# Kernel optimization log

Measured on AMD Instinct MI355X. Metric: run time of the kernel, lower is better.

Reference implementation:

```python
import jax, jax.numpy as jnp
import numpy as np

INPUT_SIZE = 128
HIDDEN_SIZE = 1024
OUTPUT_SIZE = 64
E_PROP = 0.8
E_SIZE = int(E_PROP * HIDDEN_SIZE)  # 819
I_SIZE = HIDDEN_SIZE - E_SIZE       # 205


def _make_mask():
    # rows of [+1]*E_SIZE + [-1]*I_SIZE, zero diagonal (no self-connection)
    row = np.concatenate([np.ones(E_SIZE), -np.ones(I_SIZE)]).astype(np.float32)
    mask = np.tile(row, (HIDDEN_SIZE, 1))
    np.fill_diagonal(mask, 0.0)
    return jnp.asarray(mask)


def setup_inputs() -> dict:
    key = jax.random.key(0)
    ks = jax.random.split(key, 8)
    T, B = 512, 64
    scale = 1.0 / np.sqrt(HIDDEN_SIZE)
    x = jax.random.normal(ks[0], (T, B, INPUT_SIZE), dtype=jnp.float32)
    w_ih = jax.random.normal(ks[1], (HIDDEN_SIZE, INPUT_SIZE), dtype=jnp.float32) / np.sqrt(INPUT_SIZE)
    b_ih = jax.random.uniform(ks[2], (HIDDEN_SIZE,), minval=-scale, maxval=scale, dtype=jnp.float32)
    w_hh = jax.random.normal(ks[3], (HIDDEN_SIZE, HIDDEN_SIZE), dtype=jnp.float32) * scale
    # mimic reset_parameters: shrink excitatory columns by e_size/i_size ratio
    w_hh = w_hh.at[:, :E_SIZE].divide(E_SIZE / I_SIZE)
    b_hh = jax.random.uniform(ks[4], (HIDDEN_SIZE,), minval=-scale, maxval=scale, dtype=jnp.float32)
    w_fc = jax.random.normal(ks[5], (OUTPUT_SIZE, E_SIZE), dtype=jnp.float32) / np.sqrt(E_SIZE)
    b_fc = jax.random.uniform(ks[6], (OUTPUT_SIZE,), minval=-scale, maxval=scale, dtype=jnp.float32)
    # NOTE: RNN.__init__ hard-codes alpha = 1 regardless of the value passed in.
    alpha = jnp.array([1.0], dtype=jnp.float32)
    mask = _make_mask()
    return {"x": x, "w_ih": w_ih, "b_ih": b_ih, "w_hh": w_hh, "b_hh": b_hh,
            "w_fc": w_fc, "b_fc": b_fc, "alpha": alpha, "mask": mask}


def reference(x, w_ih, b_ih, w_hh, b_hh, w_fc, b_fc, alpha, mask):
    # x: (T, B, I). Precompute input projection for all timesteps (one big GEMM).
    inp_proj = jnp.einsum('tbi,hi->tbh', x, w_ih) + b_ih  # (T, B, H)
    # effective E-I weight: sign-constrained, zero diagonal; constant across steps
    eff_w = jnp.abs(w_hh) * mask                           # (H, H)
    a = alpha[0]
    B = x.shape[1]
    state0 = jnp.zeros((B, HIDDEN_SIZE), dtype=x.dtype)
    out0 = jnp.zeros((B, HIDDEN_SIZE), dtype=x.dtype)

    def step(carry, u_t):
        state, output = carry
        total = u_t + output @ eff_w.T + b_hh             # (B, H)
        state = a * (total - state) + state               # alpha blend (sigma_rec = 0)
        output = jnp.tanh(state)
        return (state, output), output

    _, rnn_activity = jax.lax.scan(step, (state0, out0), inp_proj)  # (T, B, H)
    rnn_e = rnn_activity[:, :, :E_SIZE]                   # excitatory readout only
    out = jnp.einsum('tbe,oe->tbo', rnn_e, w_fc) + b_fc   # (T, B, O)
    return out, rnn_activity
```

## Files before the change

kernel.cpp:

```cpp
#include <hip/hip_runtime.h>
#include <cmath>

#define T_STEPS 512
#define BATCH   64
#define HID     1024
#define INSZ    128
#define ESZ     819
#define OSZ     64

#define WS_EFFW   0
#define WS_WIHT   1048576
#define WS_HIST   1179648
#define WS_BADJ   34734080
#define WS_WFCP   34742272

typedef float f32x4 __attribute__((ext_vector_type(4)));

__global__ void prep_effw(const float* __restrict__ w_hh, const float* __restrict__ mask,
                          float* __restrict__ eff) {
    const int i = (blockIdx.x * 256 + threadIdx.x) * 4;
    const float4 w = *(const float4*)(w_hh + i);
    const float4 m = *(const float4*)(mask + i);
    float4 r;
    r.x = fabsf(w.x) * m.x; r.y = fabsf(w.y) * m.y;
    r.z = fabsf(w.z) * m.z; r.w = fabsf(w.w) * m.w;
    *(float4*)(eff + i) = r;
}

__global__ void prep_wihT(const float* __restrict__ w_ih, float* __restrict__ w_ihT) {
    const int idx = blockIdx.x * 256 + threadIdx.x;
    const int i = idx >> 10, h = idx & 1023;
    w_ihT[idx] = w_ih[h * INSZ + i];
}

__global__ void prep_wfc(const float* __restrict__ w_fc, const float* __restrict__ b_fc,
                         float* __restrict__ w_fcp, float* __restrict__ badj) {
    __shared__ float red[256];
    const int o = blockIdx.x, tid = threadIdx.x;
    float s = 0.f;
    for (int e = tid; e < 820; e += 256) {
        const float w = (e < ESZ) ? w_fc[o * ESZ + e] : 0.f;
        w_fcp[o * 820 + e] = w;
        s += w;
    }
    red[tid] = s;
    __syncthreads();
    for (int st = 128; st; st >>= 1) {
        if (tid < st) red[tid] += red[tid + st];
        __syncthreads();
    }
    if (tid == 0) badj[o] = b_fc[o] - 2.0f * red[0];
}

__global__ void inp_proj(const float* __restrict__ x, const float* __restrict__ w_ihT,
                         const float* __restrict__ b_ih, float* __restrict__ u) {
    __shared__ float xs[INSZ * 64];
    const int t = blockIdx.x, tid = threadIdx.x;
    const float* xt = x + (size_t)t * BATCH * INSZ;
    for (int k = tid * 4; k < BATCH * INSZ; k += 1024) {
        const float4 v = *(const float4*)(xt + k);
        const int b = k >> 7, i = k & 127;
        xs[(i + 0) * 64 + b] = v.x; xs[(i + 1) * 64 + b] = v.y;
        xs[(i + 2) * 64 + b] = v.z; xs[(i + 3) * 64 + b] = v.w;
    }
    __syncthreads();
    for (int hp = 0; hp < 2; ++hp) {
        const int h = hp * 512 + tid * 2;
        const float bi0 = b_ih[h], bi1 = b_ih[h + 1];
        for (int b0 = 0; b0 < 64; b0 += 8) {
            float acc0[8], acc1[8];
#pragma unroll
            for (int bb = 0; bb < 8; ++bb) { acc0[bb] = 0.f; acc1[bb] = 0.f; }
#pragma unroll 4
            for (int i = 0; i < INSZ; ++i) {
                const float2 w2 = *(const float2*)(w_ihT + i * 1024 + h);
                const float4 xa = *(const float4*)(xs + i * 64 + b0);
                const float4 xb = *(const float4*)(xs + i * 64 + b0 + 4);
                const float xv[8] = {xa.x, xa.y, xa.z, xa.w, xb.x, xb.y, xb.z, xb.w};
#pragma unroll
                for (int bb = 0; bb < 8; ++bb) {
                    acc0[bb] = fmaf(w2.x, xv[bb], acc0[bb]);
                    acc1[bb] = fmaf(w2.y, xv[bb], acc1[bb]);
                }
            }
#pragma unroll
            for (int bb = 0; bb < 8; ++bb) {
                float2 r; r.x = acc0[bb] + bi0; r.y = acc1[bb] + bi1;
                *(float2*)(u + ((size_t)(b0 + bb) * T_STEPS + t) * 1024 + h) = r;
            }
        }
    }
}

#define LOAD8(SFX)                                                       \
    asm volatile("global_load_dwordx4 %0, %8, off" SFX "\n\t"            \
                 "global_load_dwordx4 %1, %8, off offset:16" SFX "\n\t"  \
                 "global_load_dwordx4 %2, %8, off offset:32" SFX "\n\t"  \
                 "global_load_dwordx4 %3, %8, off offset:48" SFX "\n\t"  \
                 "global_load_dwordx4 %4, %8, off offset:64" SFX "\n\t"  \
                 "global_load_dwordx4 %5, %8, off offset:80" SFX "\n\t"  \
                 "global_load_dwordx4 %6, %8, off offset:96" SFX "\n\t"  \
                 "global_load_dwordx4 %7, %8, off offset:112" SFX "\n\t" \
                 "s_waitcnt vmcnt(0)"                                    \
                 : "=&v"(v0), "=&v"(v1), "=&v"(v2), "=&v"(v3),           \
                   "=&v"(v4), "=&v"(v5), "=&v"(v6), "=&v"(v7)            \
                 : "v"(src) : "memory")

__device__ __forceinline__ float vmin4f(f32x4 v) {
    return fminf(fminf(v[0], v[1]), fminf(v[2], v[3]));
}

#define MIN32()                                                              \
    fminf(fminf(fminf(vmin4f(v0), vmin4f(v1)), fminf(vmin4f(v2), vmin4f(v3))), \
          fminf(fminf(vmin4f(v4), vmin4f(v5)), fminf(vmin4f(v6), vmin4f(v7))))

__global__ void __launch_bounds__(256, 1)
rnn_scan(const float* __restrict__ eff_w, const float* __restrict__ u,
         const float* __restrict__ b_hh, const float* __restrict__ alpha,
         float* __restrict__ hist) {
    extern __shared__ float smem[];
    float* w_s = smem;
    float* pp  = smem + 32768;
    const int tid = threadIdx.x, wg = blockIdx.x;
    const int bg = wg & 7, hgrp = wg >> 3;
    const int h0 = hgrp << 5, b0 = bg << 3;

    float rsum = 0.f;
    {
        const int hl = tid >> 3, grp = hl >> 2, l4 = hl & 3;
        const int j0 = (tid & 7) << 7;
        const float* wrow = eff_w + (size_t)(h0 + hl) * 1024;
        for (int j = j0; j < j0 + 128; j += 4) {
            const float4 w4 = *(const float4*)(wrow + j);
            w_s[((j + 0) << 5) + (((grp + j + 0) & 7) << 2) + l4] = w4.x;
            w_s[((j + 1) << 5) + (((grp + j + 1) & 7) << 2) + l4] = w4.y;
            w_s[((j + 2) << 5) + (((grp + j + 2) & 7) << 2) + l4] = w4.z;
            w_s[((j + 3) << 5) + (((grp + j + 3) & 7) << 2) + l4] = w4.w;
            rsum += (w4.x + w4.y) + (w4.z + w4.w);
        }
    }
    rsum += __shfl_xor(rsum, 1);
    rsum += __shfl_xor(rsum, 2);
    rsum += __shfl_xor(rsum, 4);

    const float a = alpha[0];
    const int r_hl = tid >> 3, r_b = tid & 7;
    const int rh = h0 + r_hl, rb = b0 + r_b;
    const float bias0 = b_hh[rh];
    const float bias_eff = bias0 - 2.0f * rsum;
    const size_t u_base = ((size_t)rb * T_STEPS) * 1024 + rh;
    float* const my_hist = hist + ((size_t)rb * T_STEPS) * 1024 + rh;
    const int hp = tid >> 5, jc = tid & 31;
    const int sb = tid >> 5, sj = (tid & 31) << 5;
    const float* const src_base = hist + ((size_t)(b0 + sb) * T_STEPS) * 1024 + sj;
    const int rot = tid & 7;
    float state = 0.f;
    __syncthreads();

    for (int t = 0; t < T_STEPS; ++t) {
        const float uval = u[u_base + ((size_t)t << 10)];
        float red = 0.f;
        if (t > 0) {
            f32x4 v0, v1, v2, v3, v4, v5, v6, v7;
            const float* src = src_base + ((size_t)(t - 1) << 10);
            LOAD8(" sc0");
            float mn = MIN32();
            while (!(mn >= 1.0f)) {
                __builtin_amdgcn_s_sleep(1);
                LOAD8(" sc0 sc1");
                mn = MIN32();
            }
            float* dst = pp + (sb << 10) + sj;
            *(f32x4*)(dst + (((rot + 0) & 7) << 2)) = v0;
            *(f32x4*)(dst + (((rot + 1) & 7) << 2)) = v1;
            *(f32x4*)(dst + (((rot + 2) & 7) << 2)) = v2;
            *(f32x4*)(dst + (((rot + 3) & 7) << 2)) = v3;
            *(f32x4*)(dst + (((rot + 4) & 7) << 2)) = v4;
            *(f32x4*)(dst + (((rot + 5) & 7) << 2)) = v5;
            *(f32x4*)(dst + (((rot + 6) & 7) << 2)) = v6;
            *(f32x4*)(dst + (((rot + 7) & 7) << 2)) = v7;
            __syncthreads();

            float acc[4][8];
#pragma unroll
            for (int i = 0; i < 4; ++i)
#pragma unroll
                for (int b = 0; b < 8; ++b) acc[i][b] = 0.f;
#pragma unroll 2
            for (int jj = 0; jj < 32; ++jj) {
                const int j = (jj << 5) + jc;
                const f32x4 wv = *(const f32x4*)&w_s[(j << 5) + (((hp + j) & 7) << 2)];
                const int phij = (jj << 5) + ((((jj * 9) + (jc >> 2)) & 7) << 2) + (jc & 3);
                float pv[8];
#pragma unroll
                for (int b = 0; b < 8; ++b) pv[b] = pp[(b << 10) + phij];
#pragma unroll
                for (int b = 0; b < 8; ++b) {
                    acc[0][b] = fmaf(wv[0], pv[b], acc[0][b]);
                    acc[1][b] = fmaf(wv[1], pv[b], acc[1][b]);
                    acc[2][b] = fmaf(wv[2], pv[b], acc[2][b]);
                    acc[3][b] = fmaf(wv[3], pv[b], acc[3][b]);
                }
            }
            __syncthreads();
#pragma unroll
            for (int i = 0; i < 4; ++i)
#pragma unroll
                for (int b = 0; b < 8; ++b) {
                    const int oo = ((hp << 2) + i) * 8 + b;
                    pp[(oo << 5) + ((jc + oo) & 31)] = acc[i][b];
                }
            __syncthreads();
#pragma unroll
            for (int k = 0; k < 32; ++k)
                red += pp[(tid << 5) + ((k + tid) & 31)];
        }
        const float tot = uval + red + ((t > 0) ? bias_eff : bias0);
        state = fmaf(a, tot - state, state);
        const float ov = tanhf(state);
        __hip_atomic_store(my_hist + ((size_t)t << 10), ov + 2.0f, __ATOMIC_RELAXED,
                           __HIP_MEMORY_SCOPE_AGENT);
        __syncthreads();
    }
}

__global__ void copy_act(const float* __restrict__ hist, float* __restrict__ act) {
    const int t = blockIdx.x >> 6, b = blockIdx.x & 63;
    const float* src = hist + ((size_t)b * T_STEPS + t) * 1024 + threadIdx.x * 4;
    float* dst = act + ((size_t)t * BATCH + b) * 1024 + threadIdx.x * 4;
    float4 v = *(const float4*)src;
    v.x -= 2.0f; v.y -= 2.0f; v.z -= 2.0f; v.w -= 2.0f;
    *(float4*)dst = v;
}

__global__ void fc_out(const float* __restrict__ hist, const float* __restrict__ w_fcp,
                       const float* __restrict__ badj, float* __restrict__ out0) {
    __shared__ float hs[16 * 820];
    const int t = blockIdx.x >> 2, bq = blockIdx.x & 3, tid = threadIdx.x;
    const int b0 = bq << 4;
    for (int r = 0; r < 16; ++r) {
        const float* src = hist + ((size_t)(b0 + r) * T_STEPS + t) * 1024;
        for (int e = tid; e < 820; e += 256) hs[r * 820 + e] = (e < ESZ) ? src[e] : 0.f;
    }
    __syncthreads();
    const int bb = tid >> 4, ol = tid & 15;
    float acc[4] = {0.f, 0.f, 0.f, 0.f};
    const float* hrow = hs + bb * 820;
    for (int e = 0; e < 820; e += 4) {
        const float4 hv = *(const float4*)(hrow + e);
#pragma unroll
        for (int k = 0; k < 4; ++k) {
            const float4 wv = *(const float4*)(w_fcp + (size_t)(ol + (k << 4)) * 820 + e);
            acc[k] += hv.x * wv.x + hv.y * wv.y + hv.z * wv.z + hv.w * wv.w;
        }
    }
    const int b = b0 + bb;
#pragma unroll
    for (int k = 0; k < 4; ++k) {
        const int o = ol + (k << 4);
        out0[((size_t)t * BATCH + b) * OSZ + o] = acc[k] + badj[o];
    }
}

extern "C" void kernel_launch(void* const* d_in, const int* in_sizes, int n_in,
                              void* d_out, int out_size, void* d_ws, size_t ws_size,
                              hipStream_t stream) {
    const float* x     = (const float*)d_in[0];
    const float* w_ih  = (const float*)d_in[1];
    const float* b_ih  = (const float*)d_in[2];
    const float* w_hh  = (const float*)d_in[3];
    const float* b_hh  = (const float*)d_in[4];
    const float* w_fc  = (const float*)d_in[5];
    const float* b_fc  = (const float*)d_in[6];
    const float* alpha = (const float*)d_in[7];
    const float* mask  = (const float*)d_in[8];

    float* out  = (float*)d_out;
    float* out0 = out;
    float* act  = out + (size_t)T_STEPS * BATCH * OSZ;

    float* ws     = (float*)d_ws;
    float* eff_w  = ws + WS_EFFW;
    float* w_ihT  = ws + WS_WIHT;
    float* hist   = ws + WS_HIST;
    float* badj   = ws + WS_BADJ;
    float* w_fcp  = ws + WS_WFCP;
    float* u      = act;

    hipMemsetAsync(hist, 0, (size_t)BATCH * T_STEPS * HID * sizeof(float), stream);
    prep_effw<<<1024, 256, 0, stream>>>(w_hh, mask, eff_w);
    prep_wihT<<<512, 256, 0, stream>>>(w_ih, w_ihT);
    prep_wfc<<<64, 256, 0, stream>>>(w_fc, b_fc, w_fcp, badj);
    inp_proj<<<512, 256, 0, stream>>>(x, w_ihT, b_ih, u);

    hipFuncSetAttribute(reinterpret_cast<const void*>(rnn_scan),
                        hipFuncAttributeMaxDynamicSharedMemorySize, 163840);
    void* args[] = {(void*)&eff_w, (void*)&u, (void*)&b_hh, (void*)&alpha, (void*)&hist};
    hipLaunchCooperativeKernel(reinterpret_cast<const void*>(rnn_scan),
                               dim3(256), dim3(256), args, 163840, stream);

    copy_act<<<32768, 256, 0, stream>>>(hist, act);
    fc_out<<<2048, 256, 0, stream>>>(hist, w_fcp, badj, out0);
}
```

Baseline: 4.953 ms.

## Split previous-step state polling into four chunks overlapped with the matvec

Per-step polling of the previous hidden state is split into four 256-column chunks. Each chunk's load is issued early, the next chunk is prefetched while the current one feeds the FMA loop, and each workgroup starts at a staggered chunk offset. The aim is to hide cross-workgroup flag-polling latency behind compute and let work start before the whole previous state is ready. The cost is four extra barriers per step and a more intricate, fragile inline-asm wait sequence.

Result: faster. 4.177 ms (-15.7%).

```diff
diff --git a/kernel.cpp b/kernel.cpp
--- a/kernel.cpp
+++ b/kernel.cpp
@@ -92,27 +92,22 @@
     }
 }
 
-#define LOAD8(SFX)                                                       \
-    asm volatile("global_load_dwordx4 %0, %8, off" SFX "\n\t"            \
-                 "global_load_dwordx4 %1, %8, off offset:16" SFX "\n\t"  \
-                 "global_load_dwordx4 %2, %8, off offset:32" SFX "\n\t"  \
-                 "global_load_dwordx4 %3, %8, off offset:48" SFX "\n\t"  \
-                 "global_load_dwordx4 %4, %8, off offset:64" SFX "\n\t"  \
-                 "global_load_dwordx4 %5, %8, off offset:80" SFX "\n\t"  \
-                 "global_load_dwordx4 %6, %8, off offset:96" SFX "\n\t"  \
-                 "global_load_dwordx4 %7, %8, off offset:112" SFX "\n\t" \
-                 "s_waitcnt vmcnt(0)"                                    \
-                 : "=&v"(v0), "=&v"(v1), "=&v"(v2), "=&v"(v3),           \
-                   "=&v"(v4), "=&v"(v5), "=&v"(v6), "=&v"(v7)            \
-                 : "v"(src) : "memory")
-
-__device__ __forceinline__ float vmin4f(f32x4 v) {
-    return fminf(fminf(v[0], v[1]), fminf(v[2], v[3]));
-}
-
-#define MIN32()                                                              \
-    fminf(fminf(fminf(vmin4f(v0), vmin4f(v1)), fminf(vmin4f(v2), vmin4f(v3))), \
-          fminf(fminf(vmin4f(v4), vmin4f(v5)), fminf(vmin4f(v6), vmin4f(v7))))
+#define ISSUE2(VA, VB, SRC)                                               \
+    asm volatile("global_load_dwordx4 %0, %2, off sc0\n\t"                \
+                 "global_load_dwordx4 %1, %2, off offset:512 sc0"         \
+                 : "=&v"(VA), "=&v"(VB) : "v"(SRC) : "memory")
+#define WAIT2(VA, VB)                                                     \
+    asm volatile("s_waitcnt vmcnt(0)" : "+v"(VA), "+v"(VB) :: "memory")
+#define RELOAD2(VA, VB, SRC)                                              \
+    asm volatile("global_load_dwordx4 %0, %2, off sc0 sc1\n\t"            \
+                 "global_load_dwordx4 %1, %2, off offset:512 sc0 sc1\n\t" \
+                 "s_waitcnt vmcnt(0)"                                     \
+                 : "=&v"(VA), "=&v"(VB) : "v"(SRC) : "memory")
+
+__device__ __forceinline__ float min8f(f32x4 x, f32x4 y) {
+    return fminf(fminf(fminf(x[0], x[1]), fminf(x[2], x[3])),
+                 fminf(fminf(y[0], y[1]), fminf(y[2], y[3])));
+}
 
 __global__ void __launch_bounds__(256, 1)
 rnn_scan(const float* __restrict__ eff_w, const float* __restrict__ u,
@@ -151,56 +146,62 @@
     const size_t u_base = ((size_t)rb * T_STEPS) * 1024 + rh;
     float* const my_hist = hist + ((size_t)rb * T_STEPS) * 1024 + rh;
     const int hp = tid >> 5, jc = tid & 31;
-    const int sb = tid >> 5, sj = (tid & 31) << 5;
-    const float* const src_base = hist + ((size_t)(b0 + sb) * T_STEPS) * 1024 + sj;
-    const int rot = tid & 7;
+    const int b_s = tid >> 5, q = tid & 31;
+    const float* const sbase = hist + ((size_t)(b0 + b_s) * T_STEPS) * 1024 + (q << 2);
+    const int s1 = ((q & 7) + (q >> 3)) & 7;
+    const int s2 = (s1 + 4) & 7;
+    const int ppA = (b_s << 10) + ((q >> 3) << 5) + (s1 << 2);
+    const int ppB = (b_s << 10) + 128 + ((q >> 3) << 5) + (s2 << 2);
+    const int cbase = ((hgrp >> 3) + 1) & 3;
     float state = 0.f;
+    f32x4 vA, vB;
     __syncthreads();
 
     for (int t = 0; t < T_STEPS; ++t) {
         const float uval = u[u_base + ((size_t)t << 10)];
         float red = 0.f;
         if (t > 0) {
-            f32x4 v0, v1, v2, v3, v4, v5, v6, v7;
-            const float* src = src_base + ((size_t)(t - 1) << 10);
-            LOAD8(" sc0");
-            float mn = MIN32();
-            while (!(mn >= 1.0f)) {
-                __builtin_amdgcn_s_sleep(1);
-                LOAD8(" sc0 sc1");
-                mn = MIN32();
-            }
-            float* dst = pp + (sb << 10) + sj;
-            *(f32x4*)(dst + (((rot + 0) & 7) << 2)) = v0;
-            *(f32x4*)(dst + (((rot + 1) & 7) << 2)) = v1;
-            *(f32x4*)(dst + (((rot + 2) & 7) << 2)) = v2;
-            *(f32x4*)(dst + (((rot + 3) & 7) << 2)) = v3;
-            *(f32x4*)(dst + (((rot + 4) & 7) << 2)) = v4;
-            *(f32x4*)(dst + (((rot + 5) & 7) << 2)) = v5;
-            *(f32x4*)(dst + (((rot + 6) & 7) << 2)) = v6;
-            *(f32x4*)(dst + (((rot + 7) & 7) << 2)) = v7;
-            __syncthreads();
-
+            const float* srow = sbase + ((size_t)(t - 1) << 10);
             float acc[4][8];
 #pragma unroll
             for (int i = 0; i < 4; ++i)
 #pragma unroll
                 for (int b = 0; b < 8; ++b) acc[i][b] = 0.f;
-#pragma unroll 2
-            for (int jj = 0; jj < 32; ++jj) {
-                const int j = (jj << 5) + jc;
-                const f32x4 wv = *(const f32x4*)&w_s[(j << 5) + (((hp + j) & 7) << 2)];
-                const int phij = (jj << 5) + ((((jj * 9) + (jc >> 2)) & 7) << 2) + (jc & 3);
-                float pv[8];
-#pragma unroll
-                for (int b = 0; b < 8; ++b) pv[b] = pp[(b << 10) + phij];
-#pragma unroll
-                for (int b = 0; b < 8; ++b) {
-                    acc[0][b] = fmaf(wv[0], pv[b], acc[0][b]);
-                    acc[1][b] = fmaf(wv[1], pv[b], acc[1][b]);
-                    acc[2][b] = fmaf(wv[2], pv[b], acc[2][b]);
-                    acc[3][b] = fmaf(wv[3], pv[b], acc[3][b]);
+
+            int cc = cbase;
+            for (int k = 0; k < 4; ++k) {
+                {
+                    const float* sc = srow + (cc << 8);
+                    WAIT2(vA, vB);
+                    float mn = min8f(vA, vB);
+                    while (!(mn >= 1.0f)) {
+                        __builtin_amdgcn_s_sleep(1);
+                        RELOAD2(vA, vB, sc);
+                        mn = min8f(vA, vB);
+                    }
+                    *(f32x4*)(pp + (cc << 8) + ppA) = vA;
+                    *(f32x4*)(pp + (cc << 8) + ppB) = vB;
                 }
+                __syncthreads();
+                if (k < 3) { const float* nsrc = srow + ((((cc + 1) & 3)) << 8); ISSUE2(vA, vB, nsrc); }
+#pragma unroll
+                for (int l = 0; l < 8; ++l) {
+                    const int jjg = (cc << 3) + l;
+                    const int j = (jjg << 5) + jc;
+                    const f32x4 wv = *(const f32x4*)&w_s[(j << 5) + (((hp + j) & 7) << 2)];
+                    const int phij = (jjg << 5) + ((((jc >> 2) + jjg) & 7) << 2) + (jc & 3);
+                    float pv[8];
+#pragma unroll
+                    for (int b = 0; b < 8; ++b) pv[b] = pp[(b << 10) + phij];
+#pragma unroll
+                    for (int b = 0; b < 8; ++b) {
+                        acc[0][b] = fmaf(wv[0], pv[b], acc[0][b]);
+                        acc[1][b] = fmaf(wv[1], pv[b], acc[1][b]);
+                        acc[2][b] = fmaf(wv[2], pv[b], acc[2][b]);
+                        acc[3][b] = fmaf(wv[3], pv[b], acc[3][b]);
+                    }
+                }
+                cc = (cc + 1) & 3;
             }
             __syncthreads();
 #pragma unroll
@@ -220,6 +221,7 @@
         const float ov = tanhf(state);
         __hip_atomic_store(my_hist + ((size_t)t << 10), ov + 2.0f, __ATOMIC_RELAXED,
                            __HIP_MEMORY_SCOPE_AGENT);
+        { const float* nsrc = sbase + ((size_t)t << 10) + (cbase << 8); ISSUE2(vA, vB, nsrc); }
         __syncthreads();
     }
 }
```
